# Kernel optimization log

Hardware: AMD Instinct MI355X
Metric: run time of the kernel (lower is better)

The kernel has to match this reference:

```python
import jax, jax.numpy as jnp
import numpy as np

N_NODES = 100000
N_EDGES = 800000
D_MODEL = 128
N_HEAD = 8
LN_EPS = 1e-6


def setup_inputs() -> dict:
    key = jax.random.key(0)
    ks = jax.random.split(key, 6)
    embeds = jax.random.normal(ks[0], (N_NODES, D_MODEL), dtype=jnp.float32)
    # xavier_uniform bound for square [d, d] matrix: sqrt(6 / (d + d))
    bound = float(np.sqrt(6.0 / (D_MODEL + D_MODEL)))
    qW = jax.random.uniform(ks[1], (D_MODEL, D_MODEL), minval=-bound, maxval=bound, dtype=jnp.float32)
    kW = jax.random.uniform(ks[2], (D_MODEL, D_MODEL), minval=-bound, maxval=bound, dtype=jnp.float32)
    vW = jax.random.uniform(ks[3], (D_MODEL, D_MODEL), minval=-bound, maxval=bound, dtype=jnp.float32)
    ln_gamma = jnp.ones((D_MODEL,), dtype=jnp.float32)
    ln_beta = jnp.zeros((D_MODEL,), dtype=jnp.float32)
    edge_index = jax.random.randint(ks[4], (2, N_EDGES), 0, N_NODES, dtype=jnp.int64)
    return {"embeds": embeds, "qW": qW, "kW": kW, "vW": vW,
            "ln_gamma": ln_gamma, "ln_beta": ln_beta, "edge_index": edge_index}


def reference(embeds, qW, kW, vW, ln_gamma, ln_beta, edge_index):
    rows = edge_index[0]  # destination (softmax segment) indices, [E]
    cols = edge_index[1]  # source indices, [E]
    n_nodes, d_model = embeds.shape
    n_edges = rows.shape[0]
    head = N_HEAD
    d_head = d_model // head

    row_e = embeds[rows]                      # [E, d]
    col_e = embeds[cols]                      # [E, d]
    q = (row_e @ qW).reshape(n_edges, head, d_head)
    k = (col_e @ kW).reshape(n_edges, head, d_head)
    v = (col_e @ vW).reshape(n_edges, head, d_head)

    att = jnp.einsum('ehd,ehd->eh', q, k)     # [E, h]
    att = jnp.clip(att, -10.0, 10.0)
    exp_att = jnp.exp(att)

    # segment-softmax normalization over destination node
    att_norm = jax.ops.segment_sum(exp_att, rows, num_segments=n_nodes)  # [N, h]
    att = exp_att / (att_norm[rows] + 1e-8)   # [E, h]

    res_e = (att[:, :, None] * v).reshape(n_edges, d_model)              # [E, d]
    res = jax.ops.segment_sum(res_e, rows, num_segments=n_nodes)         # [N, d]
    res = res + embeds

    # LayerNorm(eps=1e-6) over last dim
    mean = jnp.mean(res, axis=-1, keepdims=True)
    var = jnp.mean((res - mean) ** 2, axis=-1, keepdims=True)
    out = (res - mean) * jax.lax.rsqrt(var + LN_EPS) * ln_gamma + ln_beta
    return out
```

## Files before the change

kernel.cpp:

```cpp
#include <hip/hip_runtime.h>
#include <hip/hip_bf16.h>

#define N_NODES 100000
#define N_EDGES 800000
#define D 128
#define NH 8
#define NB ((N_NODES + 255) / 256)
#define NBQ ((N_NODES + 63) / 64)

typedef __hip_bfloat16 bf16;
typedef __bf16 bf16x8 __attribute__((ext_vector_type(8)));
typedef float  f32x4  __attribute__((ext_vector_type(4)));

__device__ __forceinline__ unsigned short f2bu(float x) {
    bf16 b = __float2bfloat16(x);
    return *reinterpret_cast<unsigned short*>(&b);
}
__device__ __forceinline__ float bu2f(unsigned short u) {
    return __uint_as_float(((unsigned)u) << 16);
}
__device__ __forceinline__ float bfe0(unsigned u) { return __uint_as_float(u << 16); }
__device__ __forceinline__ float bfe1(unsigned u) { return __uint_as_float(u & 0xffff0000u); }

union frag_u { unsigned short u[8]; bf16x8 v; };

template<int CTRL>
__device__ __forceinline__ float dpp_add(float x) {
    int y = __builtin_amdgcn_mov_dpp(__float_as_int(x), CTRL, 0xf, 0xf, true);
    return x + __int_as_float(y);
}
__device__ __forceinline__ float red8(float x) {
    x = dpp_add<0xB1>(x);
    x = dpp_add<0x4E>(x);
    x = dpp_add<0x141>(x);
    return x;
}

__global__ __launch_bounds__(256) void prep_kernel(
    const float* __restrict__ Wq, const float* __restrict__ Wk, const float* __restrict__ Wv,
    unsigned short* __restrict__ Wf, int* __restrict__ counts, int* __restrict__ gcur)
{
    int t = blockIdx.x * 256 + threadIdx.x;
    if (t < N_NODES) counts[t] = 0;
    if (t == 0) *gcur = 0;
    if (t < 3 * 32 * 64) {
        int lane = t & 63;
        int ct   = (t >> 6) & 31;
        int mat  = t >> 11;
        int c  = ct >> 3, tt = ct & 7;
        int n  = tt * 16 + (lane & 15);
        int kb = c * 32 + (lane >> 4) * 8;
        const float* W;
        int col;
        if (mat == 0) {
            W = Wq; col = n;
        } else {
            int g = (mat - 1) * 128 + n;
            W = (g & 2) ? Wv : Wk;
            col = ((g >> 2) << 1) | (g & 1);
        }
        unsigned short* dst = Wf + (size_t)mat * 32768 + (size_t)ct * 1024 + (size_t)lane * 8;
#pragma unroll
        for (int j = 0; j < 8; ++j) {
            float w  = W[(size_t)(kb + j) * D + col];
            unsigned short hb = f2bu(w);
            float lo = w - bu2f(hb);
            dst[j]       = hb;
            dst[512 + j] = f2bu(lo);
        }
    }
}

__global__ __launch_bounds__(256) void qkv_mfma(
    const float* __restrict__ E, const unsigned short* __restrict__ Wf,
    bf16* __restrict__ Q, char* __restrict__ KVb,
    const int* __restrict__ rows, int* __restrict__ counts,
    int* __restrict__ rank)
{
    __shared__ unsigned short bsh[16384];
    const int tid  = threadIdx.x;
    const int wave = tid >> 6;
    const int lane = tid & 63;
    const int r0w  = blockIdx.x * 64 + wave * 16;

    {
        int e0 = (blockIdx.x * 256 + tid) * 2;
        if (e0 < N_EDGES) {
            int2 r2 = *reinterpret_cast<const int2*>(rows + e0);
            int2 rk;
            rk.x = atomicAdd(&counts[r2.x], 1);
            rk.y = atomicAdd(&counts[r2.y], 1);
            *reinterpret_cast<int2*>(rank + e0) = rk;
        }
    }

    const int am = lane & 15;
    const int aq = lane >> 4;

    frag_u ahi[4], alo[4];
    {
        int row = r0w + am;
        if (row >= N_NODES) row = N_NODES - 1;
        const float* erow = E + (size_t)row * D + aq * 8;
#pragma unroll
        for (int c = 0; c < 4; ++c) {
            float4 e0 = *reinterpret_cast<const float4*>(erow + c * 32);
            float4 e1 = *reinterpret_cast<const float4*>(erow + c * 32 + 4);
            float ef[8] = {e0.x, e0.y, e0.z, e0.w, e1.x, e1.y, e1.z, e1.w};
#pragma unroll
            for (int j = 0; j < 8; ++j) {
                unsigned short hb = f2bu(ef[j]);
                ahi[c].u[j] = hb;
                alo[c].u[j] = f2bu(ef[j] - bu2f(hb));
            }
        }
    }

#pragma unroll
    for (int mat = 0; mat < 3; ++mat) {
        f32x4 acc[8];
#pragma unroll
        for (int t = 0; t < 8; ++t)
            acc[t] = (f32x4){0.f, 0.f, 0.f, 0.f};

        const unsigned short* wm = Wf + (size_t)mat * 32768;

#pragma unroll
        for (int half = 0; half < 2; ++half) {
            __syncthreads();
            const uint4* src = reinterpret_cast<const uint4*>(wm + half * 16384);
            uint4* dstv = reinterpret_cast<uint4*>(bsh);
#pragma unroll
            for (int k = 0; k < 8; ++k)
                dstv[k * 256 + tid] = src[k * 256 + tid];
            __syncthreads();

#pragma unroll
            for (int t = 0; t < 8; ++t) {
#pragma unroll
                for (int cc = 0; cc < 2; ++cc) {
                    const unsigned short* bp = bsh + (cc * 8 + t) * 1024 + lane * 8;
                    bf16x8 bhi = *reinterpret_cast<const bf16x8*>(bp);
                    bf16x8 blo = *reinterpret_cast<const bf16x8*>(bp + 512);
                    const int c = half * 2 + cc;
                    acc[t] = __builtin_amdgcn_mfma_f32_16x16x32_bf16(alo[c].v, bhi, acc[t], 0, 0, 0);
                    acc[t] = __builtin_amdgcn_mfma_f32_16x16x32_bf16(ahi[c].v, blo, acc[t], 0, 0, 0);
                    acc[t] = __builtin_amdgcn_mfma_f32_16x16x32_bf16(ahi[c].v, bhi, acc[t], 0, 0, 0);
                }
            }
        }
        __syncthreads();

        unsigned short* ob = bsh + wave * 2176;
#pragma unroll
        for (int t = 0; t < 8; ++t)
#pragma unroll
            for (int r = 0; r < 4; ++r)
                ob[(aq * 4 + r) * 136 + t * 16 + am] = f2bu(acc[t][r]);
        {
            const int row = lane >> 2, c4 = lane & 3;
            int grow = r0w + row;
            if (grow < N_NODES) {
                const uint4* srcb = reinterpret_cast<const uint4*>(ob + row * 136 + c4 * 32);
                uint4 d0 = srcb[0], d1 = srcb[1], d2 = srcb[2], d3 = srcb[3];
                uint4* dst;
                if (mat == 0)
                    dst = reinterpret_cast<uint4*>(Q + (size_t)grow * D + c4 * 32);
                else
                    dst = reinterpret_cast<uint4*>(KVb + ((size_t)grow << 9)
                                                   + (size_t)(mat - 1) * 256 + (size_t)c4 * 64);
                dst[0] = d0; dst[1] = d1; dst[2] = d2; dst[3] = d3;
            }
        }
    }
}

__global__ __launch_bounds__(256) void scan_one(
    const int* __restrict__ counts, int* __restrict__ offsets,
    int* __restrict__ gcur)
{
    int lane = threadIdx.x & 63;
    int n = blockIdx.x * 256 + threadIdx.x;
    int v = (n < N_NODES) ? counts[n] : 0;
    int s = v;
#pragma unroll
    for (int d = 1; d < 64; d <<= 1) {
        int t = __shfl_up(s, d, 64);
        if (lane >= d) s += t;
    }
    int tot = __shfl(s, 63, 64);
    int base = 0;
    if (lane == 0) base = atomicAdd(gcur, tot);
    base = __shfl(base, 0, 64);
    if (n < N_NODES) offsets[n] = base + s - v;
}

__global__ __launch_bounds__(256) void scatter_kernel(
    const int* __restrict__ rows, const int* __restrict__ cols,
    const int* __restrict__ rank, const int* __restrict__ offsets,
    int* __restrict__ csr_cols)
{
    int e0 = (blockIdx.x * 256 + threadIdx.x) * 4;
    if (e0 >= N_EDGES) return;
    int4 r4 = *reinterpret_cast<const int4*>(rows + e0);
    int4 k4 = *reinterpret_cast<const int4*>(rank + e0);
    int4 c4 = *reinterpret_cast<const int4*>(cols + e0);
    csr_cols[offsets[r4.x] + k4.x] = c4.x;
    csr_cols[offsets[r4.y] + k4.y] = c4.y;
    csr_cols[offsets[r4.z] + k4.z] = c4.z;
    csr_cols[offsets[r4.w] + k4.w] = c4.w;
}

__device__ __forceinline__ void edge_body(
    const char* __restrict__ KVb, int off, unsigned lane8,
    float q0, float q1, float CLIP2,
    float& acc0, float& acc1, float& nrm)
{
    uint2 kv = *reinterpret_cast<const uint2*>(KVb + (unsigned)off + lane8);
    float p = q0 * bfe0(kv.x) + q1 * bfe1(kv.x);
    p = red8(p);
    float s = __builtin_amdgcn_exp2f(fminf(fmaxf(p, -CLIP2), CLIP2));
    nrm  += s;
    acc0 += s * bfe0(kv.y);
    acc1 += s * bfe1(kv.y);
}

__global__ __launch_bounds__(256) void fused_node(
    const bf16* __restrict__ Qb, const char* __restrict__ KVb,
    const int* __restrict__ offsets, const int* __restrict__ counts,
    const int* __restrict__ csr_cols,
    const float* __restrict__ emb,
    const float* __restrict__ gamma, const float* __restrict__ beta,
    float* __restrict__ out)
{
    int n = blockIdx.x * 4 + (threadIdx.x >> 6);
    int lane = threadIdx.x & 63;

    const float L2E   = 1.44269504f;
    const float CLIP2 = 14.4269504f;

    unsigned qu = *reinterpret_cast<const unsigned*>(Qb + (size_t)n * D + lane * 2);
    float q0 = bfe0(qu) * L2E, q1 = bfe1(qu) * L2E;

    int start = offsets[n];
    int cnt   = counts[n];
    unsigned lane8 = (unsigned)(lane << 3);

    float acc0a = 0.f, acc1a = 0.f, nrma = 0.f;
    float acc0b = 0.f, acc1b = 0.f, nrmb = 0.f;

    for (int base = 0; base < cnt; base += 64) {
        int m = cnt - base; if (m > 64) m = 64;
        int moff = (base + lane < cnt) ? (csr_cols[start + base + lane] << 9) : 0;
        int j = 0;
        for (; j + 7 < m; j += 8) {
            int o0 = __builtin_amdgcn_readlane(moff, j + 0);
            int o1 = __builtin_amdgcn_readlane(moff, j + 1);
            int o2 = __builtin_amdgcn_readlane(moff, j + 2);
            int o3 = __builtin_amdgcn_readlane(moff, j + 3);
            int o4 = __builtin_amdgcn_readlane(moff, j + 4);
            int o5 = __builtin_amdgcn_readlane(moff, j + 5);
            int o6 = __builtin_amdgcn_readlane(moff, j + 6);
            int o7 = __builtin_amdgcn_readlane(moff, j + 7);
            edge_body(KVb, o0, lane8, q0, q1, CLIP2, acc0a, acc1a, nrma);
            edge_body(KVb, o1, lane8, q0, q1, CLIP2, acc0b, acc1b, nrmb);
            edge_body(KVb, o2, lane8, q0, q1, CLIP2, acc0a, acc1a, nrma);
            edge_body(KVb, o3, lane8, q0, q1, CLIP2, acc0b, acc1b, nrmb);
            edge_body(KVb, o4, lane8, q0, q1, CLIP2, acc0a, acc1a, nrma);
            edge_body(KVb, o5, lane8, q0, q1, CLIP2, acc0b, acc1b, nrmb);
            edge_body(KVb, o6, lane8, q0, q1, CLIP2, acc0a, acc1a, nrma);
            edge_body(KVb, o7, lane8, q0, q1, CLIP2, acc0b, acc1b, nrmb);
        }
        for (; j + 3 < m; j += 4) {
            int o0 = __builtin_amdgcn_readlane(moff, j + 0);
            int o1 = __builtin_amdgcn_readlane(moff, j + 1);
            int o2 = __builtin_amdgcn_readlane(moff, j + 2);
            int o3 = __builtin_amdgcn_readlane(moff, j + 3);
            edge_body(KVb, o0, lane8, q0, q1, CLIP2, acc0a, acc1a, nrma);
            edge_body(KVb, o1, lane8, q0, q1, CLIP2, acc0b, acc1b, nrmb);
            edge_body(KVb, o2, lane8, q0, q1, CLIP2, acc0a, acc1a, nrma);
            edge_body(KVb, o3, lane8, q0, q1, CLIP2, acc0b, acc1b, nrmb);
        }
        for (; j < m; ++j) {
            int o0 = __builtin_amdgcn_readlane(moff, j);
            edge_body(KVb, o0, lane8, q0, q1, CLIP2, acc0a, acc1a, nrma);
        }
    }

    float nrm  = nrma + nrmb;
    float acc0 = acc0a + acc0b;
    float acc1 = acc1a + acc1b;

    float w = 1.f / (nrm + 1e-8f);
    float2 e2 = *reinterpret_cast<const float2*>(emb + (size_t)n * D + lane * 2);
    float x0 = acc0 * w + e2.x;
    float x1 = acc1 * w + e2.y;

    float s1 = x0 + x1;
    float s2 = x0 * x0 + x1 * x1;
#pragma unroll
    for (int off = 32; off; off >>= 1) {
        s1 += __shfl_xor(s1, off, 64);
        s2 += __shfl_xor(s2, off, 64);
    }
    float mean = s1 * (1.0f / 128.0f);
    float var  = fmaxf(s2 * (1.0f / 128.0f) - mean * mean, 0.f);
    float rs = rsqrtf(var + 1e-6f);

    float d0 = x0 - mean, d1 = x1 - mean;
    float2 g2 = *reinterpret_cast<const float2*>(gamma + lane * 2);
    float2 b2 = *reinterpret_cast<const float2*>(beta + lane * 2);
    float2 o2 = make_float2(d0 * rs * g2.x + b2.x, d1 * rs * g2.y + b2.y);
    *reinterpret_cast<float2*>(out + (size_t)n * D + lane * 2) = o2;
}

extern "C" void kernel_launch(void* const* d_in, const int* in_sizes, int n_in,
                              void* d_out, int out_size, void* d_ws, size_t ws_size,
                              hipStream_t stream)
{
    const float* emb   = (const float*)d_in[0];
    const float* qW    = (const float*)d_in[1];
    const float* kW    = (const float*)d_in[2];
    const float* vW    = (const float*)d_in[3];
    const float* gamma = (const float*)d_in[4];
    const float* beta  = (const float*)d_in[5];
    const int*   eidx  = (const int*)d_in[6];
    const int*   rows  = eidx;
    const int*   cols  = eidx + N_EDGES;
    float* out = (float*)d_out;

    const size_t ND = (size_t)N_NODES * D;
    bf16* Qb  = (bf16*)d_ws;
    char* KVb = (char*)(Qb + ND);
    int* counts     = (int*)(KVb + (size_t)N_NODES * 512);
    int* offsets    = counts + N_NODES;
    int* rank       = offsets + N_NODES;
    int* csr_cols   = rank + N_EDGES;
    unsigned short* Wf = (unsigned short*)(csr_cols + N_EDGES);
    int* gcur       = (int*)(Wf + 3 * 32768);

    prep_kernel<<<NB, 256, 0, stream>>>(qW, kW, vW, Wf, counts, gcur);
    qkv_mfma<<<NBQ, 256, 0, stream>>>(emb, Wf, Qb, KVb, rows, counts, rank);
    scan_one<<<NB, 256, 0, stream>>>(counts, offsets, gcur);
    scatter_kernel<<<(N_EDGES / 4 + 255) / 256, 256, 0, stream>>>(rows, cols, rank, offsets, csr_cols);
    fused_node<<<(N_NODES + 3) / 4, 256, 0, stream>>>(
        Qb, KVb, offsets, counts, csr_cols, emb, gamma, beta, out);
}
```

Before: 276.9 us.

## Split QKV projection across blocks per matrix and double rows per wave

```diff
diff --git a/kernel.cpp b/kernel.cpp
--- a/kernel.cpp
+++ b/kernel.cpp
@@ -6,7 +6,7 @@
 #define D 128
 #define NH 8
 #define NB ((N_NODES + 255) / 256)
-#define NBQ ((N_NODES + 63) / 64)
+#define NBQ2 ((N_NODES + 127) / 128)
 
 typedef __hip_bfloat16 bf16;
 typedef __bf16 bf16x8 __attribute__((ext_vector_type(8)));
@@ -81,7 +81,9 @@
     const int tid  = threadIdx.x;
     const int wave = tid >> 6;
     const int lane = tid & 63;
-    const int r0w  = blockIdx.x * 64 + wave * 16;
+    const int mat    = blockIdx.x % 3;
+    const int rowblk = blockIdx.x / 3;
+    const int r0w  = rowblk * 128 + wave * 32;
 
     {
         int e0 = (blockIdx.x * 256 + tid) * 2;
@@ -97,9 +99,10 @@
     const int am = lane & 15;
     const int aq = lane >> 4;
 
-    frag_u ahi[4], alo[4];
-    {
-        int row = r0w + am;
+    frag_u ahi[2][4], alo[2][4];
+#pragma unroll
+    for (int rt = 0; rt < 2; ++rt) {
+        int row = r0w + rt * 16 + am;
         if (row >= N_NODES) row = N_NODES - 1;
         const float* erow = E + (size_t)row * D + aq * 8;
 #pragma unroll
@@ -110,67 +113,70 @@
 #pragma unroll
             for (int j = 0; j < 8; ++j) {
                 unsigned short hb = f2bu(ef[j]);
-                ahi[c].u[j] = hb;
-                alo[c].u[j] = f2bu(ef[j] - bu2f(hb));
+                ahi[rt][c].u[j] = hb;
+                alo[rt][c].u[j] = f2bu(ef[j] - bu2f(hb));
             }
         }
     }
 
-#pragma unroll
-    for (int mat = 0; mat < 3; ++mat) {
-        f32x4 acc[8];
-#pragma unroll
-        for (int t = 0; t < 8; ++t)
-            acc[t] = (f32x4){0.f, 0.f, 0.f, 0.f};
-
-        const unsigned short* wm = Wf + (size_t)mat * 32768;
-
-#pragma unroll
-        for (int half = 0; half < 2; ++half) {
-            __syncthreads();
-            const uint4* src = reinterpret_cast<const uint4*>(wm + half * 16384);
-            uint4* dstv = reinterpret_cast<uint4*>(bsh);
-#pragma unroll
-            for (int k = 0; k < 8; ++k)
-                dstv[k * 256 + tid] = src[k * 256 + tid];
-            __syncthreads();
-
-#pragma unroll
-            for (int t = 0; t < 8; ++t) {
-#pragma unroll
-                for (int cc = 0; cc < 2; ++cc) {
-                    const unsigned short* bp = bsh + (cc * 8 + t) * 1024 + lane * 8;
-                    bf16x8 bhi = *reinterpret_cast<const bf16x8*>(bp);
-                    bf16x8 blo = *reinterpret_cast<const bf16x8*>(bp + 512);
-                    const int c = half * 2 + cc;
-                    acc[t] = __builtin_amdgcn_mfma_f32_16x16x32_bf16(alo[c].v, bhi, acc[t], 0, 0, 0);
-                    acc[t] = __builtin_amdgcn_mfma_f32_16x16x32_bf16(ahi[c].v, blo, acc[t], 0, 0, 0);
-                    acc[t] = __builtin_amdgcn_mfma_f32_16x16x32_bf16(ahi[c].v, bhi, acc[t], 0, 0, 0);
+    f32x4 acc[8][2];
+#pragma unroll
+    for (int t = 0; t < 8; ++t)
+#pragma unroll
+        for (int rt = 0; rt < 2; ++rt)
+            acc[t][rt] = (f32x4){0.f, 0.f, 0.f, 0.f};
+
+    const unsigned short* wm = Wf + (size_t)mat * 32768;
+
+#pragma unroll
+    for (int half = 0; half < 2; ++half) {
+        __syncthreads();
+        const uint4* src = reinterpret_cast<const uint4*>(wm + half * 16384);
+        uint4* dstv = reinterpret_cast<uint4*>(bsh);
+#pragma unroll
+        for (int k = 0; k < 8; ++k)
+            dstv[k * 256 + tid] = src[k * 256 + tid];
+        __syncthreads();
+
+#pragma unroll
+        for (int t = 0; t < 8; ++t) {
+#pragma unroll
+            for (int cc = 0; cc < 2; ++cc) {
+                const unsigned short* bp = bsh + (cc * 8 + t) * 1024 + lane * 8;
+                bf16x8 bhi = *reinterpret_cast<const bf16x8*>(bp);
+                bf16x8 blo = *reinterpret_cast<const bf16x8*>(bp + 512);
+                const int c = half * 2 + cc;
+#pragma unroll
+                for (int rt = 0; rt < 2; ++rt) {
+                    acc[t][rt] = __builtin_amdgcn_mfma_f32_16x16x32_bf16(alo[rt][c].v, bhi, acc[t][rt], 0, 0, 0);
+                    acc[t][rt] = __builtin_amdgcn_mfma_f32_16x16x32_bf16(ahi[rt][c].v, blo, acc[t][rt], 0, 0, 0);
+                    acc[t][rt] = __builtin_amdgcn_mfma_f32_16x16x32_bf16(ahi[rt][c].v, bhi, acc[t][rt], 0, 0, 0);
                 }
             }
         }
-        __syncthreads();
-
-        unsigned short* ob = bsh + wave * 2176;
+    }
+    __syncthreads();
+
+    unsigned short* ob = bsh + wave * 2176;
+#pragma unroll
+    for (int rt = 0; rt < 2; ++rt) {
 #pragma unroll
         for (int t = 0; t < 8; ++t)
 #pragma unroll
             for (int r = 0; r < 4; ++r)
-                ob[(aq * 4 + r) * 136 + t * 16 + am] = f2bu(acc[t][r]);
-        {
-            const int row = lane >> 2, c4 = lane & 3;
-            int grow = r0w + row;
-            if (grow < N_NODES) {
-                const uint4* srcb = reinterpret_cast<const uint4*>(ob + row * 136 + c4 * 32);
-                uint4 d0 = srcb[0], d1 = srcb[1], d2 = srcb[2], d3 = srcb[3];
-                uint4* dst;
-                if (mat == 0)
-                    dst = reinterpret_cast<uint4*>(Q + (size_t)grow * D + c4 * 32);
-                else
-                    dst = reinterpret_cast<uint4*>(KVb + ((size_t)grow << 9)
-                                                   + (size_t)(mat - 1) * 256 + (size_t)c4 * 64);
-                dst[0] = d0; dst[1] = d1; dst[2] = d2; dst[3] = d3;
-            }
+                ob[(aq * 4 + r) * 136 + t * 16 + am] = f2bu(acc[t][rt][r]);
+        const int row = lane >> 2, c4 = lane & 3;
+        int grow = r0w + rt * 16 + row;
+        if (grow < N_NODES) {
+            const uint4* srcb = reinterpret_cast<const uint4*>(ob + row * 136 + c4 * 32);
+            uint4 d0 = srcb[0], d1 = srcb[1], d2 = srcb[2], d3 = srcb[3];
+            uint4* dst;
+            if (mat == 0)
+                dst = reinterpret_cast<uint4*>(Q + (size_t)grow * D + c4 * 32);
+            else
+                dst = reinterpret_cast<uint4*>(KVb + ((size_t)grow << 9)
+                                               + (size_t)(mat - 1) * 256 + (size_t)c4 * 64);
+            dst[0] = d0; dst[1] = d1; dst[2] = d2; dst[3] = d3;
         }
     }
 }
@@ -340,7 +346,7 @@
     int* gcur       = (int*)(Wf + 3 * 32768);
 
     prep_kernel<<<NB, 256, 0, stream>>>(qW, kW, vW, Wf, counts, gcur);
-    qkv_mfma<<<NBQ, 256, 0, stream>>>(emb, Wf, Qb, KVb, rows, counts, rank);
+    qkv_mfma<<<3 * NBQ2, 256, 0, stream>>>(emb, Wf, Qb, KVb, rows, counts, rank);
     scan_one<<<NB, 256, 0, stream>>>(counts, offsets, gcur);
     scatter_kernel<<<(N_EDGES / 4 + 255) / 256, 256, 0, stream>>>(rows, cols, rank, offsets, csr_cols);
     fused_node<<<(N_NODES + 3) / 4, 256, 0, stream>>>(
```

Measured after the change: 284.2 us. 2.6% more time.
